# Optimization experiments

Measured on AMD Instinct MI355X. Metric: run time of the kernel, lower is better.

## Reference

```python
import jax, jax.numpy as jnp
import numpy as np

NUM_OUT_EDGES = 2
NUM_INTERMEDIATE = 2
NUM_FSM_STATES = NUM_OUT_EDGES + NUM_INTERMEDIATE  # S = 4
NUM_EDGE_TYPES = 3
NUM_VARIANTS = 4
NUM_NODE_TYPES = 8
NUM_NODES = 256
BACKTRACK_FAILS_PROB = 0.001
EDGE_PROB = 0.05  # avg degree ~ 12.8 per edge type


def setup_inputs() -> dict:
    key = jax.random.key(0)
    k1, k2, k3, k4 = jax.random.split(key, 4)
    vw = jax.random.uniform(k1, (NUM_NODES, NUM_NODES, NUM_VARIANTS))
    vw = vw / jnp.sum(vw, axis=-1, keepdims=True)  # nonneg, sums to 1 on last axis
    adjacency = (jax.random.uniform(k2, (NUM_EDGE_TYPES, NUM_NODES, NUM_NODES)) < EDGE_PROB).astype(jnp.float32)
    n_actions = NUM_EDGE_TYPES * NUM_FSM_STATES + 3  # moves + ACCEPT/BACKTRACK/FAIL
    log_routing_params = 0.5 * jax.random.normal(
        k3, (NUM_VARIANTS, NUM_NODE_TYPES, NUM_FSM_STATES, n_actions))
    node_types = jax.random.randint(k4, (NUM_NODES,), 0, NUM_NODE_TYPES)
    return {
        'variant_weights': vw,
        'adjacency': adjacency,
        'log_routing_params': log_routing_params,
        'node_types': node_types,
        'steps': 48,
    }


def _forward(variant_weights, adjacency, log_routing_params, node_types, steps):
    N = variant_weights.shape[0]
    S, T, E = NUM_FSM_STATES, NUM_EDGE_TYPES, NUM_OUT_EDGES
    dt = variant_weights.dtype

    # Row-normalized per-edge-type adjacency (uniform over typed successors;
    deg = jnp.sum(adjacency, axis=-1, keepdims=True)
    a_norm = adjacency / jnp.maximum(deg, 1.0)  # [T, N, N]

    # routing_softmax over actions; policy conditioned on (variant, node type, fsm state)
    policy = jax.nn.softmax(log_routing_params, axis=-1)  # [V, NT, S, A]
    pol_n = policy[:, node_types]                          # [V, N, S, A]

    # Mix policy variants per (start node i, current node j)
    mixed = jnp.einsum('ijv,vjsa->ijsa', variant_weights, pol_n)  # [N, N, S, A]
    p_move = mixed[..., :T * S].reshape(N, N, S, T, S)  # MOVE(edge type t, next state u)
    p_accept = mixed[..., T * S]                        # ACCEPT at current node
    p_back = mixed[..., T * S + 1]                      # BACKTRACK to start node

    # Start states: edge type e starts in fsm state e at node i (one-hot).
    eyeS = jnp.eye(S, dtype=dt)[:E]  # [E, S]
    eyeN = jnp.eye(N, dtype=dt)      # [N, N]
    dist0 = eyeS[:, None, :, None] * eyeN[None, :, None, :]  # [E, N, S, N]
    restart = dist0 * (1.0 - BACKTRACK_FAILS_PROB)

    def step(carry, _):
        dist, accept = carry  # dist: [E, N_start, S, N_cur], accept: [E, N, N]
        accept = accept + jnp.einsum('eisj,ijs->eij', dist, p_accept)
        back = jnp.einsum('eisj,ijs->ei', dist, p_back)
        tmp = jnp.einsum('eisj,ijstu->eituj', dist, p_move)   # pick edge type + next state
        moved = jnp.einsum('eituj,tjk->eiuk', tmp, a_norm)    # move along typed edges
        dist = moved + back[:, :, None, None] * restart
        return (dist, accept), None

    accept0 = jnp.zeros((E, N, N), dt)
    (dist, accept), _ = jax.lax.scan(step, (dist0, accept0), None, length=steps)
    # absorb remaining accept probability after final transition
    accept = accept + jnp.einsum('eisj,ijs->eij', dist, p_accept)
    return accept  # [num_out_edges, num_nodes, num_nodes]


def reference(variant_weights, adjacency, log_routing_params, node_types, steps):
    return _forward(variant_weights, adjacency, log_routing_params, node_types, steps)
```

## Files before the change

kernel.cpp:

```cpp
#include <hip/hip_runtime.h>
#include <hip/hip_fp16.h>

#define NN    256
#define SS    4
#define TT    3
#define VV    4
#define NTY   8
#define NAC   15
#define CAPG  48
#define CAPE  (CAPG * 2)
#define ROWB  40
#define ZROWB (NN * ROWB)
#define BUFB  (ZROWB + ROWB)
#define ZPK   ((unsigned)ZROWB | ((unsigned)ZROWB << 16))
#define GMR   16

typedef _Float16 h2v __attribute__((ext_vector_type(2)));

#if defined(__has_builtin)
#if __has_builtin(__builtin_amdgcn_fdot2)
#define HAVE_FDOT2 1
#endif
#endif

static __device__ __forceinline__ unsigned ph2(float a, float b) {
    union { __half2 h; unsigned u; } c;
    c.h = __floats2half2_rn(a, b);
    return c.u;
}
static __device__ __forceinline__ h2v bch2(unsigned u) {
    union { unsigned u; h2v h; } c; c.u = u; return c.h;
}
static __device__ __forceinline__ float2 h2f2(unsigned u) {
    union { unsigned u; __half2 h; } c; c.u = u; return __half22float2(c.h);
}

__global__ void k_setup(const float* __restrict__ adj,
                        const float* __restrict__ lrp,
                        float* __restrict__ inv_deg,
                        float* __restrict__ pol,
                        unsigned* __restrict__ epk,
                        int* __restrict__ gcnt) {
    const int b = blockIdx.x;
    const int tid = threadIdx.x;

    if (b < TT * NN) {
        __shared__ float wsum[4];
        float s = adj[(size_t)b * NN + tid];
#pragma unroll
        for (int off = 32; off > 0; off >>= 1) s += __shfl_down(s, off, 64);
        if ((tid & 63) == 0) wsum[tid >> 6] = s;
        __syncthreads();
        if (tid == 0)
            inv_deg[b] = 1.0f / fmaxf(wsum[0] + wsum[1] + wsum[2] + wsum[3], 1.0f);
    } else if (b < TT * NN + 64) {
        __shared__ int cnt[4];
        __shared__ unsigned short offs[4][CAPE + 2];
        const int c4 = (b - TT * NN) * 4;
        if (tid < 4) cnt[tid] = 0;
        __syncthreads();
#pragma unroll
        for (int t = 0; t < TT; t++) {
            const float4 a4 = *(const float4*)(adj + ((size_t)t * NN + tid) * NN + c4);
            const float av[4] = {a4.x, a4.y, a4.z, a4.w};
#pragma unroll
            for (int c = 0; c < 4; c++) {
                if (av[c] != 0.f) {
                    int idx = atomicAdd(&cnt[c], 1);
                    if (idx < CAPE) offs[c][idx] = (unsigned short)(tid * ROWB + t * 8);
                }
            }
        }
        __syncthreads();
        const int c    = tid >> 6;
        const int lane = tid & 63;
        int cc = cnt[c]; if (cc > CAPE) cc = CAPE;
        if (lane == 0 && (cc & 1)) offs[c][cc] = (unsigned short)ZROWB;
        __syncthreads();
        const int g = (cc + 1) >> 1;
        for (int gg = lane; gg < g; gg += 64)
            epk[(size_t)gg * NN + (c4 + c)] =
                (unsigned)offs[c][2 * gg] | ((unsigned)offs[c][2 * gg + 1] << 16);
        if (lane == 0) gcnt[c4 + c] = g;
    } else {
        if (tid < VV * NTY * SS) {
            float x[NAC]; float m = -3.4e38f;
#pragma unroll
            for (int a = 0; a < NAC; a++) { x[a] = lrp[tid * NAC + a]; m = fmaxf(m, x[a]); }
            float ssum = 0.f;
#pragma unroll
            for (int a = 0; a < NAC; a++) { x[a] = __expf(x[a] - m); ssum += x[a]; }
            float inv = 1.f / ssum;
#pragma unroll
            for (int a = 0; a < NAC; a++) pol[tid * NAC + a] = x[a] * inv;
        }
    }
}

__global__ void k_sort(const int* __restrict__ gcnt, int* __restrict__ perm) {
    __shared__ int base[64];
    const int tid = threadIdx.x;
    if (tid < 64) base[tid] = 0;
    __syncthreads();
    const int g = gcnt[tid] & 63;
    atomicAdd(&base[g], 1);
    __syncthreads();
    if (tid == 0) {
        int s = 0;
#pragma unroll
        for (int b = 0; b < 64; b++) { int c = base[b]; base[b] = s; s += c; }
    }
    __syncthreads();
    const int pos = atomicAdd(&base[g], 1);
    perm[pos] = tid;
}

__global__ __launch_bounds__(512, 4) void k_main(
    const float* __restrict__ vw,
    const int* __restrict__ node_types,
    const float* __restrict__ pol,
    const float* __restrict__ inv_deg,
    const unsigned* __restrict__ epk,
    const int* __restrict__ gcnt,
    const int* __restrict__ perm,
    const int* __restrict__ steps_p,
    float* __restrict__ out)
{
    const int i    = blockIdx.x & 255;
    const int e    = blockIdx.x >> 8;
    const int tid  = threadIdx.x;
    const int col  = perm[tid >> 1];
    const int h    = tid & 1;
    const int lane = tid & 63;
    const int wv   = tid >> 6;
    const int steps = steps_p[0];

    __shared__ __align__(16) char tmpb[2 * BUFB];
    __shared__ __align__(16) float backp[2][8];

    if (tid < 20) {
        int pb = tid / 10, w = tid % 10;
        ((unsigned*)(tmpb + pb * BUFB + ZROWB))[w] = 0u;
    }

    const float4 w4 = *(const float4*)(vw + ((size_t)i * NN + col) * VV);
    const float wvv[VV] = {w4.x, w4.y, w4.z, w4.w};
    const int ntj = node_types[col];
    const int ab  = h * 6;
    float pm6[SS][6], pcb[SS];
#pragma unroll
    for (int s = 0; s < SS; s++) {
        pcb[s] = 0.f;
#pragma unroll
        for (int a = 0; a < 6; a++) pm6[s][a] = 0.f;
    }
#pragma unroll
    for (int v = 0; v < VV; v++) {
        const float* pr = pol + (size_t)(v * NTY + ntj) * SS * NAC;
#pragma unroll
        for (int s = 0; s < SS; s++) {
            const float* p = pr + s * NAC;
#pragma unroll
            for (int a = 0; a < 6; a++) pm6[s][a] = fmaf(wvv[v], p[ab + a], pm6[s][a]);
            pcb[s] = fmaf(wvv[v], p[12 + h], pcb[s]);
        }
    }
    {
        float invd[TT];
#pragma unroll
        for (int t = 0; t < TT; t++) invd[t] = inv_deg[t * NN + col];
#pragma unroll
        for (int s = 0; s < SS; s++)
#pragma unroll
            for (int a = 0; a < 6; a++) pm6[s][a] *= invd[(ab + a) >> 2];
    }

    float D0 = (0 == e && col == i) ? 1.f : 0.f;
    float D1 = (1 == e && col == i) ? 1.f : 0.f;
    float D2 = 0.f, D3 = 0.f;
    float acc = 0.f;

    const int g_all = gcnt[col];
    const int ch = (g_all - h + 1) >> 1;
    int km = ch;
#pragma unroll
    for (int off = 32; off > 0; off >>= 1) {
        int o = __shfl_xor(km, off, 64);
        km = o > km ? o : km;
    }
    const int kmax = __builtin_amdgcn_readfirstlane(km);

    unsigned ep[GMR];
#pragma unroll
    for (int k = 0; k < GMR; k++) {
        unsigned pk = epk[(size_t)(2 * k + h) * NN + col];
        ep[k] = (2 * k + h < g_all) ? pk : ZPK;
    }

    const h2v S10 = {(_Float16)1.0f, (_Float16)0.0f};
    const h2v S01 = {(_Float16)0.0f, (_Float16)1.0f};
    char* const myrow0 = tmpb + col * ROWB + h * 12;

    for (int step = 0; step < steps; step++) {
        const int par = step & 1;
        char* const buf = tmpb + par * BUFB;

        float r4 = D0 * pcb[0];
        r4 = fmaf(D1, pcb[1], r4); r4 = fmaf(D2, pcb[2], r4); r4 = fmaf(D3, pcb[3], r4);
        if (h == 0) acc += r4;
        float bj = h ? r4 : 0.f;

        float tv[6];
#pragma unroll
        for (int a = 0; a < 6; a++) {
            float x = D0 * pm6[0][a];
            x = fmaf(D1, pm6[1][a], x);
            x = fmaf(D2, pm6[2][a], x);
            x = fmaf(D3, pm6[3][a], x);
            tv[a] = x;
        }
        char* const myrow = myrow0 + par * BUFB;
        *(unsigned*)(myrow)     = ph2(tv[0], tv[1]);
        *(unsigned*)(myrow + 4) = ph2(tv[2], tv[3]);
        *(unsigned*)(myrow + 8) = ph2(tv[4], tv[5]);

#pragma unroll
        for (int off = 32; off > 0; off >>= 1) bj += __shfl_down(bj, off, 64);
        if (lane == 0) backp[par][wv] = bj;

        __syncthreads();

        float d0a = 0.f, d1a = 0.f, d2a = 0.f, d3a = 0.f;
        float d0b = 0.f, d1b = 0.f, d2b = 0.f, d3b = 0.f;
#pragma unroll
        for (int kc = 0; kc < GMR; kc += 2) {
            if (kc < kmax) {
                const unsigned pkA = ep[kc];
                const unsigned pkB = ep[kc + 1];
                const uint2 qA0 = *(const uint2*)(buf + (pkA & 0xffffu));
                const uint2 qA1 = *(const uint2*)(buf + (pkA >> 16));
                const uint2 qB0 = *(const uint2*)(buf + (pkB & 0xffffu));
                const uint2 qB1 = *(const uint2*)(buf + (pkB >> 16));
#ifdef HAVE_FDOT2
                d0a = __builtin_amdgcn_fdot2(bch2(qA0.x), S10, d0a, false);
                d1a = __builtin_amdgcn_fdot2(bch2(qA0.x), S01, d1a, false);
                d2a = __builtin_amdgcn_fdot2(bch2(qA0.y), S10, d2a, false);
                d3a = __builtin_amdgcn_fdot2(bch2(qA0.y), S01, d3a, false);
                d0a = __builtin_amdgcn_fdot2(bch2(qA1.x), S10, d0a, false);
                d1a = __builtin_amdgcn_fdot2(bch2(qA1.x), S01, d1a, false);
                d2a = __builtin_amdgcn_fdot2(bch2(qA1.y), S10, d2a, false);
                d3a = __builtin_amdgcn_fdot2(bch2(qA1.y), S01, d3a, false);
                d0b = __builtin_amdgcn_fdot2(bch2(qB0.x), S10, d0b, false);
                d1b = __builtin_amdgcn_fdot2(bch2(qB0.x), S01, d1b, false);
                d2b = __builtin_amdgcn_fdot2(bch2(qB0.y), S10, d2b, false);
                d3b = __builtin_amdgcn_fdot2(bch2(qB0.y), S01, d3b, false);
                d0b = __builtin_amdgcn_fdot2(bch2(qB1.x), S10, d0b, false);
                d1b = __builtin_amdgcn_fdot2(bch2(qB1.x), S01, d1b, false);
                d2b = __builtin_amdgcn_fdot2(bch2(qB1.y), S10, d2b, false);
                d3b = __builtin_amdgcn_fdot2(bch2(qB1.y), S01, d3b, false);
#else
                float2 f0 = h2f2(qA0.x), f1 = h2f2(qA0.y), f2 = h2f2(qA1.x), f3 = h2f2(qA1.y);
                d0a += f0.x + f2.x; d1a += f0.y + f2.y;
                d2a += f1.x + f3.x; d3a += f1.y + f3.y;
                float2 g0 = h2f2(qB0.x), g1 = h2f2(qB0.y), g2 = h2f2(qB1.x), g3 = h2f2(qB1.y);
                d0b += g0.x + g2.x; d1b += g0.y + g2.y;
                d2b += g1.x + g3.x; d3b += g1.y + g3.y;
#endif
            }
        }
        for (int k = GMR; k < kmax; k++) {
            unsigned pk = epk[(size_t)(2 * k + h) * NN + col];
            pk = (2 * k + h < g_all) ? pk : ZPK;
            const uint2 q0 = *(const uint2*)(buf + (pk & 0xffffu));
            const uint2 q1 = *(const uint2*)(buf + (pk >> 16));
            float2 f0 = h2f2(q0.x), f1 = h2f2(q0.y), f2 = h2f2(q1.x), f3 = h2f2(q1.y);
            d0a += f0.x + f2.x; d1a += f0.y + f2.y;
            d2a += f1.x + f3.x; d3a += f1.y + f3.y;
        }

        float d0 = d0a + d0b, d1 = d1a + d1b, d2 = d2a + d2b, d3 = d3a + d3b;

        d0 += __shfl_xor(d0, 1, 64);
        d1 += __shfl_xor(d1, 1, 64);
        d2 += __shfl_xor(d2, 1, 64);
        d3 += __shfl_xor(d3, 1, 64);

        if (col == i) {
            const float4 b0 = *(const float4*)(&backp[par][0]);
            const float4 b1 = *(const float4*)(&backp[par][4]);
            const float back = ((b0.x + b0.y) + (b0.z + b0.w)) +
                               ((b1.x + b1.y) + (b1.z + b1.w));
            if (e == 0) d0 = fmaf(back, 0.999f, d0);
            else        d1 = fmaf(back, 0.999f, d1);
        }
        D0 = d0; D1 = d1; D2 = d2; D3 = d3;
    }

    float r4 = D0 * pcb[0];
    r4 = fmaf(D1, pcb[1], r4); r4 = fmaf(D2, pcb[2], r4); r4 = fmaf(D3, pcb[3], r4);
    if (h == 0) {
        acc += r4;
        out[((size_t)e * NN + i) * NN + col] = acc;
    }
}

extern "C" void kernel_launch(void* const* d_in, const int* in_sizes, int n_in,
                              void* d_out, int out_size, void* d_ws, size_t ws_size,
                              hipStream_t stream) {
    const float* vw  = (const float*)d_in[0];
    const float* adj = (const float*)d_in[1];
    const float* lrp = (const float*)d_in[2];
    const int* node_types = (const int*)d_in[3];
    const int* steps_p    = (const int*)d_in[4];

    float* ws       = (float*)d_ws;
    float* pol      = ws;
    float* inv_deg  = ws + 1920;
    int*   gcnt     = (int*)(ws + 2688);
    unsigned* epk   = (unsigned*)(ws + 2944);
    int*   perm     = (int*)(ws + 2944 + CAPG * NN);

    k_setup<<<TT * NN + 64 + 1, 256, 0, stream>>>(adj, lrp, inv_deg, pol, epk, gcnt);
    k_sort<<<1, 256, 0, stream>>>(gcnt, perm);
    k_main<<<2 * NN, 512, 0, stream>>>(vw, node_types, pol, inv_deg, epk, gcnt,
                                       perm, steps_p, (float*)d_out);
}
```

Measured before the change: 163.4 us.

## Store LDS rows in permuted rank order and bank-spread edge offsets

The main kernel now indexes its shared-memory row buffer by sorted rank instead of original column, so the sort kernel remaps every edge offset through the inverse permutation. Each column's edge list is bucketed by an LDS bank key and rotated per thread, which spreads the gather reads across banks and cuts LDS bank conflicts in the inner step loop. The cost is a heavier single-block sort kernel that runs serial per-thread loops, plus extra workspace buffers.

```diff
diff --git a/kernel.cpp b/kernel.cpp
--- a/kernel.cpp
+++ b/kernel.cpp
@@ -39,8 +39,8 @@
                         const float* __restrict__ lrp,
                         float* __restrict__ inv_deg,
                         float* __restrict__ pol,
-                        unsigned* __restrict__ epk,
-                        int* __restrict__ gcnt) {
+                        unsigned short* __restrict__ eoff,
+                        int* __restrict__ ecnt) {
     const int b = blockIdx.x;
     const int tid = threadIdx.x;
 
@@ -55,7 +55,7 @@
             inv_deg[b] = 1.0f / fmaxf(wsum[0] + wsum[1] + wsum[2] + wsum[3], 1.0f);
     } else if (b < TT * NN + 64) {
         __shared__ int cnt[4];
-        __shared__ unsigned short offs[4][CAPE + 2];
+        __shared__ unsigned short raw[4][CAPE];
         const int c4 = (b - TT * NN) * 4;
         if (tid < 4) cnt[tid] = 0;
         __syncthreads();
@@ -67,7 +67,7 @@
             for (int c = 0; c < 4; c++) {
                 if (av[c] != 0.f) {
                     int idx = atomicAdd(&cnt[c], 1);
-                    if (idx < CAPE) offs[c][idx] = (unsigned short)(tid * ROWB + t * 8);
+                    if (idx < CAPE) raw[c][idx] = (unsigned short)((tid << 2) | t);
                 }
             }
         }
@@ -75,13 +75,9 @@
         const int c    = tid >> 6;
         const int lane = tid & 63;
         int cc = cnt[c]; if (cc > CAPE) cc = CAPE;
-        if (lane == 0 && (cc & 1)) offs[c][cc] = (unsigned short)ZROWB;
-        __syncthreads();
-        const int g = (cc + 1) >> 1;
-        for (int gg = lane; gg < g; gg += 64)
-            epk[(size_t)gg * NN + (c4 + c)] =
-                (unsigned)offs[c][2 * gg] | ((unsigned)offs[c][2 * gg + 1] << 16);
-        if (lane == 0) gcnt[c4 + c] = g;
+        for (int j = lane; j < cc; j += 64)
+            eoff[(size_t)(c4 + c) * CAPE + j] = raw[c][j];
+        if (lane == 0) ecnt[c4 + c] = cc;
     } else {
         if (tid < VV * NTY * SS) {
             float x[NAC]; float m = -3.4e38f;
@@ -97,13 +93,21 @@
     }
 }
 
-__global__ void k_sort(const int* __restrict__ gcnt, int* __restrict__ perm) {
+__global__ void k_sort(const int* __restrict__ ecnt,
+                       const unsigned short* __restrict__ eoff,
+                       unsigned short* __restrict__ eoff2,
+                       int* __restrict__ perm,
+                       int* __restrict__ invperm,
+                       unsigned* __restrict__ epk,
+                       int* __restrict__ gcnt) {
     __shared__ int base[64];
+    __shared__ unsigned short bins[256][16];
     const int tid = threadIdx.x;
     if (tid < 64) base[tid] = 0;
     __syncthreads();
-    const int g = gcnt[tid] & 63;
-    atomicAdd(&base[g], 1);
+    const int m0 = ecnt[tid];
+    const int g0 = ((m0 + 1) >> 1) & 63;
+    atomicAdd(&base[g0], 1);
     __syncthreads();
     if (tid == 0) {
         int s = 0;
@@ -111,8 +115,50 @@
         for (int b = 0; b < 64; b++) { int c = base[b]; base[b] = s; s += c; }
     }
     __syncthreads();
-    const int pos = atomicAdd(&base[g], 1);
+    const int pos = atomicAdd(&base[g0], 1);
     perm[pos] = tid;
+    __syncthreads();
+    invperm[perm[tid]] = tid;
+    __syncthreads();
+
+    const int q   = tid;
+    const int col = perm[q];
+    const int m   = ecnt[col];
+    const unsigned short* src = eoff + (size_t)col * CAPE;
+    unsigned short* dst = eoff2 + (size_t)col * CAPE;
+
+#pragma unroll
+    for (int bp = 0; bp < 16; bp++) bins[q][bp] = 0;
+    for (int j = 0; j < m; j++) {
+        const int rt = src[j];
+        const int rr = invperm[rt >> 2], t = rt & 3;
+        bins[q][(5 * rr + t) & 15]++;
+    }
+    {
+        int s = 0;
+#pragma unroll
+        for (int bp = 0; bp < 16; bp++) { int c = bins[q][bp]; bins[q][bp] = (unsigned short)s; s += c; }
+    }
+    for (int j = 0; j < m; j++) {
+        const int rt = src[j];
+        const int rr = invperm[rt >> 2], t = rt & 3;
+        const int key = (5 * rr + t) & 15;
+        const int p = bins[q][key]++;
+        dst[p] = (unsigned short)(rr * ROWB + t * 8);
+    }
+    const int rho = ((q & 15) * m) >> 4;
+    const int G = (m + 1) >> 1;
+    for (int g = 0; g < G; g++) {
+        int p0 = 2 * g + rho;     if (p0 >= m) p0 -= m;
+        unsigned a = dst[p0];
+        unsigned bwd = (unsigned)ZROWB;
+        if (2 * g + 1 < m) {
+            int p1 = 2 * g + 1 + rho; if (p1 >= m) p1 -= m;
+            bwd = dst[p1];
+        }
+        epk[(size_t)g * NN + col] = a | (bwd << 16);
+    }
+    gcnt[col] = G;
 }
 
 __global__ __launch_bounds__(512, 4) void k_main(
@@ -129,7 +175,8 @@
     const int i    = blockIdx.x & 255;
     const int e    = blockIdx.x >> 8;
     const int tid  = threadIdx.x;
-    const int col  = perm[tid >> 1];
+    const int rank = tid >> 1;
+    const int col  = perm[rank];
     const int h    = tid & 1;
     const int lane = tid & 63;
     const int wv   = tid >> 6;
@@ -199,7 +246,7 @@
 
     const h2v S10 = {(_Float16)1.0f, (_Float16)0.0f};
     const h2v S01 = {(_Float16)0.0f, (_Float16)1.0f};
-    char* const myrow0 = tmpb + col * ROWB + h * 12;
+    char* const myrow0 = tmpb + rank * ROWB + h * 12;
 
     for (int step = 0; step < steps; step++) {
         const int par = step & 1;
@@ -313,15 +360,19 @@
     const int* node_types = (const int*)d_in[3];
     const int* steps_p    = (const int*)d_in[4];
 
-    float* ws       = (float*)d_ws;
-    float* pol      = ws;
-    float* inv_deg  = ws + 1920;
-    int*   gcnt     = (int*)(ws + 2688);
-    unsigned* epk   = (unsigned*)(ws + 2944);
-    int*   perm     = (int*)(ws + 2944 + CAPG * NN);
-
-    k_setup<<<TT * NN + 64 + 1, 256, 0, stream>>>(adj, lrp, inv_deg, pol, epk, gcnt);
-    k_sort<<<1, 256, 0, stream>>>(gcnt, perm);
+    float* ws            = (float*)d_ws;
+    float* pol           = ws;
+    float* inv_deg       = ws + 1920;
+    int*   gcnt          = (int*)(ws + 2688);
+    unsigned* epk        = (unsigned*)(ws + 2944);
+    int*   perm          = (int*)(ws + 2944 + CAPG * NN);
+    int*   invperm       = (int*)(ws + 2944 + CAPG * NN + 256);
+    int*   ecnt          = (int*)(ws + 2944 + CAPG * NN + 512);
+    unsigned short* eoff  = (unsigned short*)(ws + 2944 + CAPG * NN + 768);
+    unsigned short* eoff2 = eoff + (size_t)CAPE * NN;
+
+    k_setup<<<TT * NN + 64 + 1, 256, 0, stream>>>(adj, lrp, inv_deg, pol, eoff, ecnt);
+    k_sort<<<1, 256, 0, stream>>>(ecnt, eoff, eoff2, perm, invperm, epk, gcnt);
     k_main<<<2 * NN, 512, 0, stream>>>(vw, node_types, pol, inv_deg, epk, gcnt,
                                        perm, steps_p, (float*)d_out);
 }
```

New measurement: 192.4 us. 1.18x slower.
